# Performance work log

Measured on AMD Instinct MI355X. Metric: run time of the kernel, lower is better.

## Reference

```python
import jax, jax.numpy as jnp
import numpy as np

N = 50000
F = 96
E = 800000
H = 2
DEPTH = 3
LEAKY_ALPHA = 0.2  # tf.nn.leaky_relu default


def setup_inputs() -> dict:
    key = jax.random.key(0)
    k1, k2, k3, k4, k5, k6 = jax.random.split(key, 6)
    node_f = jax.random.normal(k1, (N, F), dtype=jnp.float32)
    rows = jax.random.randint(k2, (E,), 0, N, dtype=jnp.int64)
    cols = jax.random.randint(k3, (E,), 0, N, dtype=jnp.int64)
    adj_idx = jnp.stack([rows, cols], axis=-1)[None]  # [1, E, 2]
    diag = jnp.arange(N, dtype=jnp.int64)
    adj_self_idx = jnp.stack([diag, diag], axis=-1)  # [N, 2] self loops
    adj_self_val = jax.random.uniform(k4, (N,), dtype=jnp.float32)
    attn_self_k = jax.random.normal(k5, (H, F), dtype=jnp.float32) * 0.05
    attn_neigh_k = jax.random.normal(k6, (H, F), dtype=jnp.float32) * 0.05
    return {"node_f": node_f, "adj_idx": adj_idx, "adj_self_idx": adj_self_idx,
            "adj_self_val": adj_self_val, "attn_self_k": attn_self_k,
            "attn_neigh_k": attn_neigh_k}


def _segment_softmax(scores, seg, n):
    # softmax over the nonzero entries of each row (tf.sparse_softmax semantics)
    m = jax.ops.segment_max(scores, seg, num_segments=n)
    ex = jnp.exp(scores - m[seg])
    denom = jax.ops.segment_sum(ex, seg, num_segments=n)
    return ex / denom[seg]


def reference(node_f, adj_idx, adj_self_idx, adj_self_val, attn_self_k, attn_neigh_k):
    rows = adj_idx[0, :, 0]
    cols = adj_idx[0, :, 1]
    s_rows = adj_self_idx[:, 0]
    s_cols = adj_self_idx[:, 1]
    # features = adj_self @ node_f (sparse matmul)
    features = jax.ops.segment_sum(adj_self_val[:, None] * node_f[s_cols],
                                   s_rows, num_segments=N)
    features = jax.nn.relu(features)
    outputs = [features]
    for _ in range(DEPTH):
        def head_fn(a_s, a_n, feats=features):
            e_self = feats @ a_s    # [N]
            e_neigh = feats @ a_n   # [N]
            scores = jax.nn.leaky_relu(e_self[rows] + e_neigh[cols], LEAKY_ALPHA)
            att = _segment_softmax(scores, rows, N)  # [E]
            return jax.ops.segment_sum(att[:, None] * feats[cols], rows,
                                       num_segments=N)  # [N, F]
        heads = jax.vmap(head_fn)(attn_self_k, attn_neigh_k)  # [H, N, F]
        features = jax.nn.relu(jnp.mean(heads, axis=0))
        outputs.append(features)
    return jnp.concatenate(outputs, axis=-1)  # [N, F*(DEPTH+1)]
```

## Files before the change

kernel.cpp:

```cpp
#include <hip/hip_runtime.h>
#include <math.h>

#define NN 50000
#define FF 96
#define EE 800000
#define OF 384
#define GB 3125
#define FBU 48
#define CAP 64
#define NB 196
#define BCAP 4608
#define CHUNK 4082

__device__ __forceinline__ float grp_sum(float v) {
    for (int m = 8; m >= 1; m >>= 1) v += __shfl_xor(v, m, 64);
    return v;
}
__device__ __forceinline__ float grp_max(float v) {
    for (int m = 8; m >= 1; m >>= 1) v = fmaxf(v, __shfl_xor(v, m, 64));
    return v;
}
__device__ __forceinline__ float lrelu(float x) { return x > 0.f ? x : 0.2f * x; }
__device__ __forceinline__ void online_upd(float s, float& m, float& d) {
    float nm = fmaxf(m, s);
    d = d * __expf(m - nm) + __expf(s - nm);
    m = nm;
}
__device__ __forceinline__ float bf_lo(unsigned u) { return __uint_as_float(u << 16); }
__device__ __forceinline__ float bf_hi(unsigned u) { return __uint_as_float(u & 0xffff0000u); }
__device__ __forceinline__ unsigned pack_bf(float a, float b) {
    unsigned ua = __float_as_uint(a), ub = __float_as_uint(b);
    ua = ua + 0x7fffu + ((ua >> 16) & 1u);
    ub = ub + 0x7fffu + ((ub >> 16) & 1u);
    return (ua >> 16) | (ub & 0xffff0000u);
}

__device__ __forceinline__ float grp_dot8(const float* a,
                                          const float* __restrict__ kf, int lg) {
    float s = 0.f;
    if (lg < 12) {
        float4 w0 = ((const float4*)kf)[2 * lg];
        float4 w1 = ((const float4*)kf)[2 * lg + 1];
        s = a[0] * w0.x + a[1] * w0.y + a[2] * w0.z + a[3] * w0.w +
            a[4] * w1.x + a[5] * w1.y + a[6] * w1.z + a[7] * w1.w;
    }
    return grp_sum(s);
}

template<int BF>
__global__ __launch_bounds__(256) void l0_phase1(const float* __restrict__ node_f,
                                                 const int* __restrict__ sidx,
                                                 const float* __restrict__ sval,
                                                 float* __restrict__ out,
                                                 unsigned* __restrict__ fb,
                                                 const float* __restrict__ ks,
                                                 const float* __restrict__ kn,
                                                 float2* __restrict__ ass,
                                                 float2* __restrict__ ann,
                                                 const int2* __restrict__ idx2,
                                                 int* __restrict__ bfill,
                                                 unsigned* __restrict__ buckets) {
    __shared__ int cnt[NB], basearr[NB], ofs[NB];
    int tid = threadIdx.x;
    if (blockIdx.x >= GB) {
        int p = blockIdx.x - GB;
        int start = p * CHUNK, end = min(start + CHUNK, EE);
        if (tid < NB) { cnt[tid] = 0; ofs[tid] = 0; }
        __syncthreads();
        for (int e = start + tid; e < end; e += 256)
            atomicAdd(&cnt[idx2[e].x >> 8], 1);
        __syncthreads();
        if (tid < NB)
            basearr[tid] = cnt[tid] ? atomicAdd(&bfill[tid], cnt[tid]) : 0;
        __syncthreads();
        for (int e = start + tid; e < end; e += 256) {
            int2 q = idx2[e];
            int b = q.x >> 8;
            int slot = basearr[b] + atomicAdd(&ofs[b], 1);
            if (slot < BCAP)
                buckets[(size_t)b * BCAP + slot] =
                    ((unsigned)(q.x & 255) << 16) | (unsigned)q.y;
        }
        return;
    }
    int g = tid >> 4, lg = tid & 15;
    int n = blockIdx.x * 16 + g;
    if (n >= NN) return;
    int sr = sidx[2 * n];
    int sc = sidx[2 * n + 1];
    float v = sval[n];
    float a[8] = {0.f, 0.f, 0.f, 0.f, 0.f, 0.f, 0.f, 0.f};
    if (lg < 12) {
        const float4* xr4 = (const float4*)(node_f + (size_t)sc * FF);
        float4 x0 = xr4[2 * lg], x1 = xr4[2 * lg + 1];
        a[0] = fmaxf(v * x0.x, 0.f); a[1] = fmaxf(v * x0.y, 0.f);
        a[2] = fmaxf(v * x0.z, 0.f); a[3] = fmaxf(v * x0.w, 0.f);
        a[4] = fmaxf(v * x1.x, 0.f); a[5] = fmaxf(v * x1.y, 0.f);
        a[6] = fmaxf(v * x1.z, 0.f); a[7] = fmaxf(v * x1.w, 0.f);
        float4* op4 = (float4*)(out + (size_t)sr * OF);
        op4[2 * lg]     = make_float4(a[0], a[1], a[2], a[3]);
        op4[2 * lg + 1] = make_float4(a[4], a[5], a[6], a[7]);
        if (BF) {
            uint4 p;
            p.x = pack_bf(a[0], a[1]); p.y = pack_bf(a[2], a[3]);
            p.z = pack_bf(a[4], a[5]); p.w = pack_bf(a[6], a[7]);
            ((uint4*)(fb + (size_t)sr * FBU))[lg] = p;
        }
    }
    float p0 = grp_dot8(a, ks, lg);
    float p1 = grp_dot8(a, ks + FF, lg);
    float p2 = grp_dot8(a, kn, lg);
    float p3 = grp_dot8(a, kn + FF, lg);
    if (lg == 0) {
        ass[sr] = make_float2(p0, p1);
        ann[sr] = make_float2(p2, p3);
    }
}

__global__ __launch_bounds__(256) void bucket2csr(const int* __restrict__ bfill,
                                                  const unsigned* __restrict__ buckets,
                                                  int* __restrict__ fill,
                                                  unsigned short* __restrict__ csr) {
    __shared__ unsigned short lcsr[256 * CAP];
    __shared__ int lfill[256];
    int tid = threadIdx.x, b = blockIdx.x;
    lfill[tid] = 0;
    __syncthreads();
    int cnt = min(bfill[b], BCAP);
    for (int i = tid; i < cnt; i += 256) {
        unsigned u = buckets[(size_t)b * BCAP + i];
        int lr = u >> 16;
        int s = atomicAdd(&lfill[lr], 1);
        if (s < CAP) lcsr[lr * CAP + s] = (unsigned short)(u & 0xffffu);
    }
    __syncthreads();
    const uint4* src = (const uint4*)lcsr;
    uint4* dst = (uint4*)(csr + (size_t)b * 256 * CAP);
    for (int i = tid; i < 256 * CAP / 8; i += 256) dst[i] = src[i];
    int r = b * 256 + tid;
    if (r < NN) fill[r] = min(lfill[tid], CAP);
}

template<int BF>
__device__ __forceinline__ void agg_chunk(float cj, int colj, int nj, int gbase,
                                          const float* __restrict__ feats,
                                          const unsigned* __restrict__ fb, int lg,
                                          float* a) {
#pragma unroll 8
    for (int k = 0; k < nj; ++k) {
        float cc = __shfl(cj, gbase + k, 64);
        int col  = __shfl(colj, gbase + k, 64);
        if (lg < 12) {
            if (BF) {
                uint4 q = ((const uint4*)(fb + (size_t)col * FBU))[lg];
                a[0] += cc * bf_lo(q.x); a[1] += cc * bf_hi(q.x);
                a[2] += cc * bf_lo(q.y); a[3] += cc * bf_hi(q.y);
                a[4] += cc * bf_lo(q.z); a[5] += cc * bf_hi(q.z);
                a[6] += cc * bf_lo(q.w); a[7] += cc * bf_hi(q.w);
            } else {
                const float4* vp = (const float4*)(feats + (size_t)col * OF);
                float4 v0 = vp[2 * lg], v1 = vp[2 * lg + 1];
                a[0] += cc * v0.x; a[1] += cc * v0.y;
                a[2] += cc * v0.z; a[3] += cc * v0.w;
                a[4] += cc * v1.x; a[5] += cc * v1.y;
                a[6] += cc * v1.z; a[7] += cc * v1.w;
            }
        }
    }
}

template<int BF>
__global__ __launch_bounds__(256) void gat_layer(float* __restrict__ out, int l,
                                                 const int* __restrict__ fill,
                                                 const unsigned short* __restrict__ csr,
                                                 const float2* __restrict__ ass,
                                                 const float2* __restrict__ ann,
                                                 const unsigned* __restrict__ fb_in,
                                                 unsigned* __restrict__ fb_out,
                                                 const float* __restrict__ ks,
                                                 const float* __restrict__ kn,
                                                 float2* __restrict__ ass_out,
                                                 float2* __restrict__ ann_out,
                                                 int write_dots) {
    int tid = threadIdx.x;
    int g = tid >> 4, lg = tid & 15;
    int gbase = (g & 3) * 16;
    int r = blockIdx.x * 16 + g;
    if (r >= NN) return;
    int deg = fill[r];
    const unsigned short* crow = csr + (size_t)r * CAP;
    const float* feats = out + l * FF;
    float2 as_r = ass[r];

    float m0 = -1e30f, m1 = -1e30f, d0 = 0.f, d1 = 0.f;
    int   c0col = 0, c1col = 0;
    float c0s0 = -1e30f, c0s1 = -1e30f, c1s0 = -1e30f, c1s1 = -1e30f;
    if (lg < deg) {
        int c = crow[lg];
        float2 an = ann[c];
        c0col = c;
        c0s0 = lrelu(as_r.x + an.x);
        c0s1 = lrelu(as_r.y + an.y);
        online_upd(c0s0, m0, d0);
        online_upd(c0s1, m1, d1);
    }
    if (deg > 16) {
        int j = 16 + lg;
        if (j < deg) {
            int c = crow[j];
            float2 an = ann[c];
            c1col = c;
            c1s0 = lrelu(as_r.x + an.x);
            c1s1 = lrelu(as_r.y + an.y);
            online_upd(c1s0, m0, d0);
            online_upd(c1s1, m1, d1);
        }
        for (int j0 = 32; j0 < deg; j0 += 16) {
            int jj = j0 + lg;
            if (jj < deg) {
                int c = crow[jj];
                float2 an = ann[c];
                online_upd(lrelu(as_r.x + an.x), m0, d0);
                online_upd(lrelu(as_r.y + an.y), m1, d1);
            }
        }
    }
    float M0 = grp_max(m0), M1 = grp_max(m1);
    d0 = grp_sum(d0 * __expf(m0 - M0));
    d1 = grp_sum(d1 * __expf(m1 - M1));
    float inv0 = d0 > 0.f ? 0.5f / d0 : 0.f;
    float inv1 = d1 > 0.f ? 0.5f / d1 : 0.f;

    float a[8] = {0.f, 0.f, 0.f, 0.f, 0.f, 0.f, 0.f, 0.f};
    {
        float cj = __expf(c0s0 - M0) * inv0 + __expf(c0s1 - M1) * inv1;
        agg_chunk<BF>(cj, c0col, min(deg, 16), gbase, feats, fb_in, lg, a);
    }
    if (deg > 16) {
        float cj = __expf(c1s0 - M0) * inv0 + __expf(c1s1 - M1) * inv1;
        agg_chunk<BF>(cj, c1col, min(deg - 16, 16), gbase, feats, fb_in, lg, a);
        for (int j0 = 32; j0 < deg; j0 += 16) {
            float cjr = 0.f; int colr = 0;
            int jj = j0 + lg;
            if (jj < deg) {
                int c = crow[jj];
                float2 an = ann[c];
                cjr = __expf(lrelu(as_r.x + an.x) - M0) * inv0 +
                      __expf(lrelu(as_r.y + an.y) - M1) * inv1;
                colr = c;
            }
            agg_chunk<BF>(cjr, colr, min(deg - j0, 16), gbase, feats, fb_in, lg, a);
        }
    }

#pragma unroll
    for (int i = 0; i < 8; ++i) a[i] = fmaxf(a[i], 0.f);
    if (lg < 12) {
        float4* op4 = (float4*)(out + (size_t)r * OF + (l + 1) * FF);
        op4[2 * lg]     = make_float4(a[0], a[1], a[2], a[3]);
        op4[2 * lg + 1] = make_float4(a[4], a[5], a[6], a[7]);
        if (BF && fb_out) {
            uint4 p;
            p.x = pack_bf(a[0], a[1]); p.y = pack_bf(a[2], a[3]);
            p.z = pack_bf(a[4], a[5]); p.w = pack_bf(a[6], a[7]);
            ((uint4*)(fb_out + (size_t)r * FBU))[lg] = p;
        }
    }

    if (write_dots) {
        float p0 = grp_dot8(a, ks, lg);
        float p1 = grp_dot8(a, ks + FF, lg);
        float p2 = grp_dot8(a, kn, lg);
        float p3 = grp_dot8(a, kn + FF, lg);
        if (lg == 0) {
            ass_out[r] = make_float2(p0, p1);
            ann_out[r] = make_float2(p2, p3);
        }
    }
}

extern "C" void kernel_launch(void* const* d_in, const int* in_sizes, int n_in,
                              void* d_out, int out_size, void* d_ws, size_t ws_size,
                              hipStream_t stream) {
    const float* node_f  = (const float*)d_in[0];
    const int*   adj_idx = (const int*)d_in[1];
    const int*   sidx    = (const int*)d_in[2];
    const float* sval    = (const float*)d_in[3];
    const float* k_self  = (const float*)d_in[4];
    const float* k_neigh = (const float*)d_in[5];
    float* out = (float*)d_out;

    char* w = (char*)d_ws;
    auto alloc = [&](size_t bytes) {
        char* p = w;
        w += (bytes + 255) & ~(size_t)255;
        return p;
    };
    int*            fill    = (int*)alloc((size_t)NN * 4);
    unsigned short* csr     = (unsigned short*)alloc((size_t)NB * 256 * CAP * 2);
    int*            bfill   = (int*)alloc((size_t)NB * 4);
    unsigned*       buckets = (unsigned*)alloc((size_t)NB * BCAP * 4);
    float2*         ass_a   = (float2*)alloc((size_t)NN * 8);
    float2*         ann_a   = (float2*)alloc((size_t)NN * 8);
    float2*         ass_b   = (float2*)alloc((size_t)NN * 8);
    float2*         ann_b   = (float2*)alloc((size_t)NN * 8);
    unsigned*       fb_a    = (unsigned*)alloc((size_t)NN * FBU * 4);
    unsigned*       fb_b    = (unsigned*)alloc((size_t)NN * FBU * 4);
    bool bf = (size_t)(w - (char*)d_ws) <= ws_size;

    hipMemsetAsync(bfill, 0, (size_t)NB * 4, stream);

    if (bf) {
        l0_phase1<1><<<GB + NB, 256, 0, stream>>>(node_f, sidx, sval, out, fb_a,
                                                  k_self, k_neigh, ass_a, ann_a,
                                                  (const int2*)adj_idx, bfill, buckets);
        bucket2csr<<<NB, 256, 0, stream>>>(bfill, buckets, fill, csr);
        gat_layer<1><<<GB, 256, 0, stream>>>(out, 0, fill, csr, ass_a, ann_a,
                                             fb_a, fb_b, k_self, k_neigh,
                                             ass_b, ann_b, 1);
        gat_layer<1><<<GB, 256, 0, stream>>>(out, 1, fill, csr, ass_b, ann_b,
                                             fb_b, fb_a, k_self, k_neigh,
                                             ass_a, ann_a, 1);
        gat_layer<1><<<GB, 256, 0, stream>>>(out, 2, fill, csr, ass_a, ann_a,
                                             fb_a, nullptr, k_self, k_neigh,
                                             ass_b, ann_b, 0);
    } else {
        l0_phase1<0><<<GB + NB, 256, 0, stream>>>(node_f, sidx, sval, out, nullptr,
                                                  k_self, k_neigh, ass_a, ann_a,
                                                  (const int2*)adj_idx, bfill, buckets);
        bucket2csr<<<NB, 256, 0, stream>>>(bfill, buckets, fill, csr);
        gat_layer<0><<<GB, 256, 0, stream>>>(out, 0, fill, csr, ass_a, ann_a,
                                             nullptr, nullptr, k_self, k_neigh,
                                             ass_b, ann_b, 1);
        gat_layer<0><<<GB, 256, 0, stream>>>(out, 1, fill, csr, ass_b, ann_b,
                                             nullptr, nullptr, k_self, k_neigh,
                                             ass_a, ann_a, 1);
        gat_layer<0><<<GB, 256, 0, stream>>>(out, 2, fill, csr, ass_a, ann_a,
                                             nullptr, nullptr, k_self, k_neigh,
                                             ass_b, ann_b, 0);
    }
}
```

Baseline: 235.3 us.

## Process two rows per lane group and sort CSR columns by shard

Each 16-lane group in the GAT layer now handles two adjacent rows, loading both rows' column indices and scores up front and interleaving their neighbour gathers in one loop. The aim is more independent memory requests in flight per wave while halving the grid. Separately, bucket2csr now counting-sorts each row's neighbours into four column shards, so gathers within a row touch nearby addresses for better cache locality. The costs are higher register pressure, fewer blocks, and an extra pass plus atomics in the CSR build.

```diff
diff --git a/kernel.cpp b/kernel.cpp
--- a/kernel.cpp
+++ b/kernel.cpp
@@ -6,11 +6,13 @@
 #define EE 800000
 #define OF 384
 #define GB 3125
+#define GL 1563
 #define FBU 48
 #define CAP 64
 #define NB 196
 #define BCAP 4608
 #define CHUNK 4082
+#define SHARD 12500
 
 __device__ __forceinline__ float grp_sum(float v) {
     for (int m = 8; m >= 1; m >>= 1) v += __shfl_xor(v, m, 64);
@@ -122,49 +124,93 @@
                                                   int* __restrict__ fill,
                                                   unsigned short* __restrict__ csr) {
     __shared__ unsigned short lcsr[256 * CAP];
-    __shared__ int lfill[256];
+    __shared__ int lcnt[256 * 4], loff[256 * 4];
     int tid = threadIdx.x, b = blockIdx.x;
-    lfill[tid] = 0;
+#pragma unroll
+    for (int c = 0; c < 4; ++c) lcnt[tid * 4 + c] = 0;
     __syncthreads();
     int cnt = min(bfill[b], BCAP);
+    const unsigned* bp = buckets + (size_t)b * BCAP;
     for (int i = tid; i < cnt; i += 256) {
-        unsigned u = buckets[(size_t)b * BCAP + i];
-        int lr = u >> 16;
-        int s = atomicAdd(&lfill[lr], 1);
-        if (s < CAP) lcsr[lr * CAP + s] = (unsigned short)(u & 0xffffu);
+        unsigned u = bp[i];
+        atomicAdd(&lcnt[(u >> 16) * 4 + (int)((u & 0xffffu) / SHARD)], 1);
+    }
+    __syncthreads();
+    {
+        int c0 = lcnt[tid * 4], c1 = lcnt[tid * 4 + 1];
+        int c2 = lcnt[tid * 4 + 2], c3 = lcnt[tid * 4 + 3];
+        loff[tid * 4] = 0;
+        loff[tid * 4 + 1] = c0;
+        loff[tid * 4 + 2] = c0 + c1;
+        loff[tid * 4 + 3] = c0 + c1 + c2;
+        int r = b * 256 + tid;
+        if (r < NN) fill[r] = min(c0 + c1 + c2 + c3, CAP);
+        lcnt[tid * 4] = 0; lcnt[tid * 4 + 1] = 0;
+        lcnt[tid * 4 + 2] = 0; lcnt[tid * 4 + 3] = 0;
+    }
+    __syncthreads();
+    for (int i = tid; i < cnt; i += 256) {
+        unsigned u = bp[i];
+        int lr = u >> 16, col = u & 0xffffu, cls = col / SHARD;
+        int pos = loff[lr * 4 + cls] + atomicAdd(&lcnt[lr * 4 + cls], 1);
+        if (pos < CAP) lcsr[lr * CAP + pos] = (unsigned short)col;
     }
     __syncthreads();
     const uint4* src = (const uint4*)lcsr;
     uint4* dst = (uint4*)(csr + (size_t)b * 256 * CAP);
     for (int i = tid; i < 256 * CAP / 8; i += 256) dst[i] = src[i];
-    int r = b * 256 + tid;
-    if (r < NN) fill[r] = min(lfill[tid], CAP);
 }
 
 template<int BF>
-__device__ __forceinline__ void agg_chunk(float cj, int colj, int nj, int gbase,
-                                          const float* __restrict__ feats,
-                                          const unsigned* __restrict__ fb, int lg,
-                                          float* a) {
-#pragma unroll 8
-    for (int k = 0; k < nj; ++k) {
-        float cc = __shfl(cj, gbase + k, 64);
-        int col  = __shfl(colj, gbase + k, 64);
-        if (lg < 12) {
-            if (BF) {
-                uint4 q = ((const uint4*)(fb + (size_t)col * FBU))[lg];
-                a[0] += cc * bf_lo(q.x); a[1] += cc * bf_hi(q.x);
-                a[2] += cc * bf_lo(q.y); a[3] += cc * bf_hi(q.y);
-                a[4] += cc * bf_lo(q.z); a[5] += cc * bf_hi(q.z);
-                a[6] += cc * bf_lo(q.w); a[7] += cc * bf_hi(q.w);
-            } else {
-                const float4* vp = (const float4*)(feats + (size_t)col * OF);
-                float4 v0 = vp[2 * lg], v1 = vp[2 * lg + 1];
-                a[0] += cc * v0.x; a[1] += cc * v0.y;
-                a[2] += cc * v0.z; a[3] += cc * v0.w;
-                a[4] += cc * v1.x; a[5] += cc * v1.y;
-                a[6] += cc * v1.z; a[7] += cc * v1.w;
+__device__ __forceinline__ void gfma(int col, float cc, int lg,
+                                     const float* __restrict__ feats,
+                                     const unsigned* __restrict__ fb, float* a) {
+    if (lg < 12) {
+        if (BF) {
+            uint4 q = ((const uint4*)(fb + (size_t)col * FBU))[lg];
+            a[0] += cc * bf_lo(q.x); a[1] += cc * bf_hi(q.x);
+            a[2] += cc * bf_lo(q.y); a[3] += cc * bf_hi(q.y);
+            a[4] += cc * bf_lo(q.z); a[5] += cc * bf_hi(q.z);
+            a[6] += cc * bf_lo(q.w); a[7] += cc * bf_hi(q.w);
+        } else {
+            const float4* vp = (const float4*)(feats + (size_t)col * OF);
+            float4 v0 = vp[2 * lg], v1 = vp[2 * lg + 1];
+            a[0] += cc * v0.x; a[1] += cc * v0.y;
+            a[2] += cc * v0.z; a[3] += cc * v0.w;
+            a[4] += cc * v1.x; a[5] += cc * v1.y;
+            a[6] += cc * v1.z; a[7] += cc * v1.w;
+        }
+    }
+}
+
+template<int BF>
+__device__ void agg_row(int deg, float e0, float e1, int c0, int c1,
+                        const unsigned short* __restrict__ crow, float2 as_r,
+                        const float2* __restrict__ ann,
+                        float M0, float M1, float inv0, float inv1,
+                        int gbase, int lg, const float* __restrict__ feats,
+                        const unsigned* __restrict__ fb, float* a) {
+    int n0 = min(deg, 16);
+    for (int k = 0; k < n0; ++k)
+        gfma<BF>(__shfl(c0, gbase + k, 64), __shfl(e0, gbase + k, 64), lg, feats, fb, a);
+    if (deg > 16) {
+        int n1 = min(deg - 16, 16);
+        for (int k = 0; k < n1; ++k)
+            gfma<BF>(__shfl(c1, gbase + k, 64), __shfl(e1, gbase + k, 64), lg, feats, fb, a);
+        for (int j0 = 32; j0 < deg; j0 += 16) {
+            float cjr = 0.f; int colr = 0;
+            int jj = j0 + lg;
+            if (jj < deg) {
+                int c = crow[jj];
+                float2 an = ann[c];
+                cjr = __expf(lrelu(as_r.x + an.x) - M0) * inv0 +
+                      __expf(lrelu(as_r.y + an.y) - M1) * inv1;
+                colr = c;
             }
+            int nj = min(deg - j0, 16);
+            for (int k = 0; k < nj; ++k)
+                gfma<BF>(__shfl(colr, gbase + k, 64), __shfl(cjr, gbase + k, 64),
+                         lg, feats, fb, a);
         }
     }
 }
@@ -185,96 +231,139 @@
     int tid = threadIdx.x;
     int g = tid >> 4, lg = tid & 15;
     int gbase = (g & 3) * 16;
-    int r = blockIdx.x * 16 + g;
-    if (r >= NN) return;
-    int deg = fill[r];
-    const unsigned short* crow = csr + (size_t)r * CAP;
+    int rA = blockIdx.x * 32 + g * 2;
+    if (rA >= NN) return;
+    int rB = rA + 1;
+    int degA = fill[rA], degB = fill[rB];
+    const unsigned short* crA = csr + (size_t)rA * CAP;
+    const unsigned short* crB = csr + (size_t)rB * CAP;
     const float* feats = out + l * FF;
-    float2 as_r = ass[r];
-
-    float m0 = -1e30f, m1 = -1e30f, d0 = 0.f, d1 = 0.f;
-    int   c0col = 0, c1col = 0;
-    float c0s0 = -1e30f, c0s1 = -1e30f, c1s0 = -1e30f, c1s1 = -1e30f;
-    if (lg < deg) {
-        int c = crow[lg];
-        float2 an = ann[c];
-        c0col = c;
-        c0s0 = lrelu(as_r.x + an.x);
-        c0s1 = lrelu(as_r.y + an.y);
-        online_upd(c0s0, m0, d0);
-        online_upd(c0s1, m1, d1);
-    }
-    if (deg > 16) {
-        int j = 16 + lg;
-        if (j < deg) {
-            int c = crow[j];
-            float2 an = ann[c];
-            c1col = c;
-            c1s0 = lrelu(as_r.x + an.x);
-            c1s1 = lrelu(as_r.y + an.y);
-            online_upd(c1s0, m0, d0);
-            online_upd(c1s1, m1, d1);
-        }
-        for (int j0 = 32; j0 < deg; j0 += 16) {
+    float2 asA = ass[rA], asB = ass[rB];
+
+    int cA0 = 0, cB0 = 0, cA1 = 0, cB1 = 0;
+    if (lg < degA) cA0 = crA[lg];
+    if (lg < degB) cB0 = crB[lg];
+    if (16 + lg < degA) cA1 = crA[16 + lg];
+    if (16 + lg < degB) cB1 = crB[16 + lg];
+    float2 anA0 = ann[cA0], anB0 = ann[cB0];
+    float2 anA1 = ann[cA1], anB1 = ann[cB1];
+
+    float mA0 = -1e30f, mA1 = -1e30f, dA0 = 0.f, dA1 = 0.f;
+    float mB0 = -1e30f, mB1 = -1e30f, dB0 = 0.f, dB1 = 0.f;
+    float sA00 = -1e30f, sA01 = -1e30f, sA10 = -1e30f, sA11 = -1e30f;
+    float sB00 = -1e30f, sB01 = -1e30f, sB10 = -1e30f, sB11 = -1e30f;
+    if (lg < degA) {
+        sA00 = lrelu(asA.x + anA0.x); sA01 = lrelu(asA.y + anA0.y);
+        online_upd(sA00, mA0, dA0); online_upd(sA01, mA1, dA1);
+    }
+    if (16 + lg < degA) {
+        sA10 = lrelu(asA.x + anA1.x); sA11 = lrelu(asA.y + anA1.y);
+        online_upd(sA10, mA0, dA0); online_upd(sA11, mA1, dA1);
+    }
+    if (lg < degB) {
+        sB00 = lrelu(asB.x + anB0.x); sB01 = lrelu(asB.y + anB0.y);
+        online_upd(sB00, mB0, dB0); online_upd(sB01, mB1, dB1);
+    }
+    if (16 + lg < degB) {
+        sB10 = lrelu(asB.x + anB1.x); sB11 = lrelu(asB.y + anB1.y);
+        online_upd(sB10, mB0, dB0); online_upd(sB11, mB1, dB1);
+    }
+    if (degA > 32)
+        for (int j0 = 32; j0 < degA; j0 += 16) {
             int jj = j0 + lg;
-            if (jj < deg) {
-                int c = crow[jj];
-                float2 an = ann[c];
-                online_upd(lrelu(as_r.x + an.x), m0, d0);
-                online_upd(lrelu(as_r.y + an.y), m1, d1);
+            if (jj < degA) {
+                int c = crA[jj]; float2 an = ann[c];
+                online_upd(lrelu(asA.x + an.x), mA0, dA0);
+                online_upd(lrelu(asA.y + an.y), mA1, dA1);
             }
         }
-    }
-    float M0 = grp_max(m0), M1 = grp_max(m1);
-    d0 = grp_sum(d0 * __expf(m0 - M0));
-    d1 = grp_sum(d1 * __expf(m1 - M1));
-    float inv0 = d0 > 0.f ? 0.5f / d0 : 0.f;
-    float inv1 = d1 > 0.f ? 0.5f / d1 : 0.f;
-
-    float a[8] = {0.f, 0.f, 0.f, 0.f, 0.f, 0.f, 0.f, 0.f};
-    {
-        float cj = __expf(c0s0 - M0) * inv0 + __expf(c0s1 - M1) * inv1;
-        agg_chunk<BF>(cj, c0col, min(deg, 16), gbase, feats, fb_in, lg, a);
-    }
-    if (deg > 16) {
-        float cj = __expf(c1s0 - M0) * inv0 + __expf(c1s1 - M1) * inv1;
-        agg_chunk<BF>(cj, c1col, min(deg - 16, 16), gbase, feats, fb_in, lg, a);
-        for (int j0 = 32; j0 < deg; j0 += 16) {
-            float cjr = 0.f; int colr = 0;
+    if (degB > 32)
+        for (int j0 = 32; j0 < degB; j0 += 16) {
             int jj = j0 + lg;
-            if (jj < deg) {
-                int c = crow[jj];
-                float2 an = ann[c];
-                cjr = __expf(lrelu(as_r.x + an.x) - M0) * inv0 +
-                      __expf(lrelu(as_r.y + an.y) - M1) * inv1;
-                colr = c;
+            if (jj < degB) {
+                int c = crB[jj]; float2 an = ann[c];
+                online_upd(lrelu(asB.x + an.x), mB0, dB0);
+                online_upd(lrelu(asB.y + an.y), mB1, dB1);
             }
-            agg_chunk<BF>(cjr, colr, min(deg - j0, 16), gbase, feats, fb_in, lg, a);
-        }
+        }
+    float MA0 = grp_max(mA0), MA1 = grp_max(mA1);
+    float MB0 = grp_max(mB0), MB1 = grp_max(mB1);
+    dA0 = grp_sum(dA0 * __expf(mA0 - MA0));
+    dA1 = grp_sum(dA1 * __expf(mA1 - MA1));
+    dB0 = grp_sum(dB0 * __expf(mB0 - MB0));
+    dB1 = grp_sum(dB1 * __expf(mB1 - MB1));
+    float invA0 = dA0 > 0.f ? 0.5f / dA0 : 0.f;
+    float invA1 = dA1 > 0.f ? 0.5f / dA1 : 0.f;
+    float invB0 = dB0 > 0.f ? 0.5f / dB0 : 0.f;
+    float invB1 = dB1 > 0.f ? 0.5f / dB1 : 0.f;
+    float eA0 = __expf(sA00 - MA0) * invA0 + __expf(sA01 - MA1) * invA1;
+    float eA1 = __expf(sA10 - MA0) * invA0 + __expf(sA11 - MA1) * invA1;
+    float eB0 = __expf(sB00 - MB0) * invB0 + __expf(sB01 - MB1) * invB1;
+    float eB1 = __expf(sB10 - MB0) * invB0 + __expf(sB11 - MB1) * invB1;
+
+    float aA[8] = {0.f, 0.f, 0.f, 0.f, 0.f, 0.f, 0.f, 0.f};
+    float aB[8] = {0.f, 0.f, 0.f, 0.f, 0.f, 0.f, 0.f, 0.f};
+    if (degA <= 32 && degB <= 32) {
+        int dmax = max(degA, degB);
+#pragma unroll 4
+        for (int j = 0; j < dmax; ++j) {
+            if (j < degA) {
+                float cc; int col;
+                if (j < 16) { cc = __shfl(eA0, gbase + j, 64);      col = __shfl(cA0, gbase + j, 64); }
+                else        { cc = __shfl(eA1, gbase + j - 16, 64); col = __shfl(cA1, gbase + j - 16, 64); }
+                gfma<BF>(col, cc, lg, feats, fb_in, aA);
+            }
+            if (j < degB) {
+                float cc; int col;
+                if (j < 16) { cc = __shfl(eB0, gbase + j, 64);      col = __shfl(cB0, gbase + j, 64); }
+                else        { cc = __shfl(eB1, gbase + j - 16, 64); col = __shfl(cB1, gbase + j - 16, 64); }
+                gfma<BF>(col, cc, lg, feats, fb_in, aB);
+            }
+        }
+    } else {
+        agg_row<BF>(degA, eA0, eA1, cA0, cA1, crA, asA, ann, MA0, MA1,
+                    invA0, invA1, gbase, lg, feats, fb_in, aA);
+        agg_row<BF>(degB, eB0, eB1, cB0, cB1, crB, asB, ann, MB0, MB1,
+                    invB0, invB1, gbase, lg, feats, fb_in, aB);
     }
 
 #pragma unroll
-    for (int i = 0; i < 8; ++i) a[i] = fmaxf(a[i], 0.f);
+    for (int i = 0; i < 8; ++i) {
+        aA[i] = fmaxf(aA[i], 0.f);
+        aB[i] = fmaxf(aB[i], 0.f);
+    }
     if (lg < 12) {
-        float4* op4 = (float4*)(out + (size_t)r * OF + (l + 1) * FF);
-        op4[2 * lg]     = make_float4(a[0], a[1], a[2], a[3]);
-        op4[2 * lg + 1] = make_float4(a[4], a[5], a[6], a[7]);
+        float4* oA = (float4*)(out + (size_t)rA * OF + (l + 1) * FF);
+        oA[2 * lg]     = make_float4(aA[0], aA[1], aA[2], aA[3]);
+        oA[2 * lg + 1] = make_float4(aA[4], aA[5], aA[6], aA[7]);
+        float4* oB = (float4*)(out + (size_t)rB * OF + (l + 1) * FF);
+        oB[2 * lg]     = make_float4(aB[0], aB[1], aB[2], aB[3]);
+        oB[2 * lg + 1] = make_float4(aB[4], aB[5], aB[6], aB[7]);
         if (BF && fb_out) {
-            uint4 p;
-            p.x = pack_bf(a[0], a[1]); p.y = pack_bf(a[2], a[3]);
-            p.z = pack_bf(a[4], a[5]); p.w = pack_bf(a[6], a[7]);
-            ((uint4*)(fb_out + (size_t)r * FBU))[lg] = p;
+            uint4 pA, pB;
+            pA.x = pack_bf(aA[0], aA[1]); pA.y = pack_bf(aA[2], aA[3]);
+            pA.z = pack_bf(aA[4], aA[5]); pA.w = pack_bf(aA[6], aA[7]);
+            pB.x = pack_bf(aB[0], aB[1]); pB.y = pack_bf(aB[2], aB[3]);
+            pB.z = pack_bf(aB[4], aB[5]); pB.w = pack_bf(aB[6], aB[7]);
+            ((uint4*)(fb_out + (size_t)rA * FBU))[lg] = pA;
+            ((uint4*)(fb_out + (size_t)rB * FBU))[lg] = pB;
         }
     }
 
     if (write_dots) {
-        float p0 = grp_dot8(a, ks, lg);
-        float p1 = grp_dot8(a, ks + FF, lg);
-        float p2 = grp_dot8(a, kn, lg);
-        float p3 = grp_dot8(a, kn + FF, lg);
+        float pA0 = grp_dot8(aA, ks, lg);
+        float pA1 = grp_dot8(aA, ks + FF, lg);
+        float pA2 = grp_dot8(aA, kn, lg);
+        float pA3 = grp_dot8(aA, kn + FF, lg);
+        float pB0 = grp_dot8(aB, ks, lg);
+        float pB1 = grp_dot8(aB, ks + FF, lg);
+        float pB2 = grp_dot8(aB, kn, lg);
+        float pB3 = grp_dot8(aB, kn + FF, lg);
         if (lg == 0) {
-            ass_out[r] = make_float2(p0, p1);
-            ann_out[r] = make_float2(p2, p3);
+            ass_out[rA] = make_float2(pA0, pA1);
+            ann_out[rA] = make_float2(pA2, pA3);
+            ass_out[rB] = make_float2(pB0, pB1);
+            ann_out[rB] = make_float2(pB2, pB3);
         }
     }
 }
@@ -315,13 +404,13 @@
                                                   k_self, k_neigh, ass_a, ann_a,
                                                   (const int2*)adj_idx, bfill, buckets);
         bucket2csr<<<NB, 256, 0, stream>>>(bfill, buckets, fill, csr);
-        gat_layer<1><<<GB, 256, 0, stream>>>(out, 0, fill, csr, ass_a, ann_a,
+        gat_layer<1><<<GL, 256, 0, stream>>>(out, 0, fill, csr, ass_a, ann_a,
                                              fb_a, fb_b, k_self, k_neigh,
                                              ass_b, ann_b, 1);
-        gat_layer<1><<<GB, 256, 0, stream>>>(out, 1, fill, csr, ass_b, ann_b,
+        gat_layer<1><<<GL, 256, 0, stream>>>(out, 1, fill, csr, ass_b, ann_b,
                                              fb_b, fb_a, k_self, k_neigh,
                                              ass_a, ann_a, 1);
-        gat_layer<1><<<GB, 256, 0, stream>>>(out, 2, fill, csr, ass_a, ann_a,
+        gat_layer<1><<<GL, 256, 0, stream>>>(out, 2, fill, csr, ass_a, ann_a,
                                              fb_a, nullptr, k_self, k_neigh,
                                              ass_b, ann_b, 0);
     } else {
@@ -329,13 +418,13 @@
                                                   k_self, k_neigh, ass_a, ann_a,
                                                   (const int2*)adj_idx, bfill, buckets);
         bucket2csr<<<NB, 256, 0, stream>>>(bfill, buckets, fill, csr);
-        gat_layer<0><<<GB, 256, 0, stream>>>(out, 0, fill, csr, ass_a, ann_a,
+        gat_layer<0><<<GL, 256, 0, stream>>>(out, 0, fill, csr, ass_a, ann_a,
                                              nullptr, nullptr, k_self, k_neigh,
                                              ass_b, ann_b, 1);
-        gat_layer<0><<<GB, 256, 0, stream>>>(out, 1, fill, csr, ass_b, ann_b,
+        gat_layer<0><<<GL, 256, 0, stream>>>(out, 1, fill, csr, ass_b, ann_b,
                                              nullptr, nullptr, k_self, k_neigh,
                                              ass_a, ann_a, 1);
-        gat_layer<0><<<GB, 256, 0, stream>>>(out, 2, fill, csr, ass_a, ann_a,
+        gat_layer<0><<<GL, 256, 0, stream>>>(out, 2, fill, csr, ass_a, ann_a,
                                              nullptr, nullptr, k_self, k_neigh,
                                              ass_b, ann_b, 0);
     }
```

After: 260.9 us. 1.11x slower.
